# Performance work log

Hardware: AMD Instinct MI355X
Metric: run time of the kernel (lower is better)

## Reference

```python
import jax, jax.numpy as jnp
import numpy as np

N_NODES = 50000
N_EDGES = 800000
F_IN = 64
H1 = 64
H2 = 64
OUT = 8
N_GRAPHS = 128


def gcn_conv(x, W, b, src, dst, n_nodes):
    """PyG GCNConv: sym-normalized aggregation with self-loops.
    out_i = sum_{j->i} d_j^{-1/2} d_i^{-1/2} (x_j W) + d_i^{-1} (x_i W) + b
    where d includes the self-loop (+1)."""
    h = x @ W  # [N, out]
    ones = jnp.ones((src.shape[0],), dtype=x.dtype)
    deg = jnp.zeros((n_nodes,), dtype=x.dtype).at[dst].add(ones) + 1.0  # +1 self-loop
    dinv_sqrt = jax.lax.rsqrt(deg)
    norm = dinv_sqrt[src] * dinv_sqrt[dst]  # [E]
    msgs = h[src] * norm[:, None]  # [E, out] -- dominant memory traffic
    agg = jax.ops.segment_sum(msgs, dst, num_segments=n_nodes)
    agg = agg + h * (1.0 / deg)[:, None]  # self-loop term (norm = 1/d_i)
    return agg + b


def setup_inputs() -> dict:
    key = jax.random.key(0)
    ks = jax.random.split(key, 10)
    x = jax.random.normal(ks[0], (N_NODES, F_IN), dtype=jnp.float32)
    src = jax.random.randint(ks[1], (N_EDGES,), 0, N_NODES, dtype=jnp.int32)
    dst = jax.random.randint(ks[2], (N_EDGES,), 0, N_NODES, dtype=jnp.int32)
    batch = jnp.sort(jax.random.randint(ks[3], (N_NODES,), 0, N_GRAPHS, dtype=jnp.int32))
    s1 = 1.0 / np.sqrt(F_IN)
    s2 = 1.0 / np.sqrt(H1)
    s3 = 1.0 / np.sqrt(H2)
    W1 = jax.random.uniform(ks[4], (F_IN, H1), jnp.float32, -s1, s1)
    b1 = jnp.zeros((H1,), jnp.float32)
    W2 = jax.random.uniform(ks[5], (H1, H2), jnp.float32, -s2, s2)
    b2 = jnp.zeros((H2,), jnp.float32)
    Wfc = jax.random.uniform(ks[6], (H2, OUT), jnp.float32, -s3, s3)
    bfc = jax.random.uniform(ks[7], (OUT,), jnp.float32, -s3, s3)
    return {"x": x, "src": src, "dst": dst, "batch": batch,
            "W1": W1, "b1": b1, "W2": W2, "b2": b2, "Wfc": Wfc, "bfc": bfc}


def reference(x, src, dst, batch, W1, b1, W2, b2, Wfc, bfc):
    n = x.shape[0]
    h = jnp.tanh(gcn_conv(x, W1, b1, src, dst, n))  # dropout(p=0) is identity
    h = jnp.tanh(gcn_conv(h, W2, b2, src, dst, n))
    # global mean pool over graphs
    sums = jax.ops.segment_sum(h, batch, num_segments=N_GRAPHS)  # [G, H2]
    counts = jax.ops.segment_sum(jnp.ones((n,), h.dtype), batch, num_segments=N_GRAPHS)
    pooled = sums / jnp.maximum(counts, 1.0)[:, None]
    return pooled @ Wfc + bfc  # [G, OUT]
```

## Files before the change

### kernel.cpp

```cpp
#include <hip/hip_runtime.h>
#include <hip/hip_fp16.h>
#include <math.h>


#define TPB 256
#define NBIN 256
#define NBLK 256
#define MSZ  (NBIN*NBLK)
#define CAP  4608

#define ADD8(a, v) do { const __half2* _h = (const __half2*)&(v);             \
    float2 _f0 = __half22float2(_h[0]), _f1 = __half22float2(_h[1]);          \
    float2 _f2 = __half22float2(_h[2]), _f3 = __half22float2(_h[3]);          \
    a[0] += _f0.x; a[1] += _f0.y; a[2] += _f1.x; a[3] += _f1.y;               \
    a[4] += _f2.x; a[5] += _f2.y; a[6] += _f3.x; a[7] += _f3.y; } while (0)

__global__ __launch_bounds__(TPB) void k_hist_gemm(const int* __restrict__ dst, int E,
                                                   int* __restrict__ Gh, int binw,
                                                   const float* __restrict__ X,
                                                   const float* __restrict__ W,
                                                   float* __restrict__ Y, int N) {
    if (blockIdx.x < NBIN) {
        __shared__ int hist[NBIN];
        hist[threadIdx.x] = 0;
        __syncthreads();
        int chunk = (E + NBLK - 1) / NBLK;
        int start = blockIdx.x * chunk;
        int end = min(start + chunk, E);
        for (int e = start + threadIdx.x; e < end; e += TPB)
            atomicAdd(&hist[dst[e] / binw], 1);
        __syncthreads();
        Gh[threadIdx.x * NBLK + blockIdx.x] = hist[threadIdx.x];
        return;
    }
    __shared__ float4 Ws[64][16];
    for (int i = threadIdx.x; i < 64 * 16; i += TPB)
        Ws[i >> 4][i & 15] = ((const float4*)W)[i];
    __syncthreads();

    int row = (blockIdx.x - NBIN) * TPB + threadIdx.x;
    if (row >= N) return;
    float xr[64];
    const float4* xp = (const float4*)(X + (size_t)row * 64);
#pragma unroll
    for (int q = 0; q < 16; q++) {
        float4 t = xp[q];
        xr[4 * q + 0] = t.x; xr[4 * q + 1] = t.y;
        xr[4 * q + 2] = t.z; xr[4 * q + 3] = t.w;
    }
    float4 acc[16];
#pragma unroll
    for (int q = 0; q < 16; q++) acc[q] = make_float4(0.f, 0.f, 0.f, 0.f);
#pragma unroll
    for (int k = 0; k < 64; k++) {
        float xk = xr[k];
#pragma unroll
        for (int q = 0; q < 16; q++) {
            float4 w = Ws[k][q];
            acc[q].x += xk * w.x; acc[q].y += xk * w.y;
            acc[q].z += xk * w.z; acc[q].w += xk * w.w;
        }
    }
    float4* yp = (float4*)(Y + (size_t)row * 64);
#pragma unroll
    for (int q = 0; q < 16; q++) yp[q] = acc[q];
}

__global__ __launch_bounds__(1024) void k_scanA(const int* __restrict__ Gh,
                                                int* __restrict__ localex,
                                                int* __restrict__ bsum) {
    __shared__ int buf[1024];
    int i = blockIdx.x * 1024 + threadIdx.x;
    int v = Gh[i];
    buf[threadIdx.x] = v;
    __syncthreads();
#pragma unroll
    for (int off = 1; off < 1024; off <<= 1) {
        int t = (threadIdx.x >= off) ? buf[threadIdx.x - off] : 0;
        __syncthreads();
        buf[threadIdx.x] += t;
        __syncthreads();
    }
    localex[i] = buf[threadIdx.x] - v;
    if (threadIdx.x == 1023) bsum[blockIdx.x] = buf[1023];
}

__global__ __launch_bounds__(1024) void k_scanC(const int* __restrict__ localex,
                                                const int* __restrict__ bsum,
                                                int* __restrict__ Gbase,
                                                int* __restrict__ binptr, int E) {
    __shared__ int offs;
    if (threadIdx.x == 0) {
        int run = 0;
        for (int j = 0; j < (int)blockIdx.x; j++) run += bsum[j];
        offs = run;
    }
    __syncthreads();
    int i = blockIdx.x * 1024 + threadIdx.x;
    int r = localex[i] + offs;
    Gbase[i] = r;
    if ((i & (NBLK - 1)) == 0) binptr[i / NBLK] = r;
    if (i == 0) binptr[NBIN] = E;
}

__global__ __launch_bounds__(TPB) void k_binscatter(const int* __restrict__ src,
                                                    const int* __restrict__ dst,
                                                    const int* __restrict__ Gbase,
                                                    unsigned int* __restrict__ Ebin,
                                                    int E, int binw) {
    __shared__ int curs[NBIN];
    curs[threadIdx.x] = Gbase[threadIdx.x * NBLK + blockIdx.x];
    __syncthreads();
    int chunk = (E + NBLK - 1) / NBLK;
    int start = blockIdx.x * chunk;
    int end = min(start + chunk, E);
    for (int e = start + threadIdx.x; e < end; e += TPB) {
        int d = dst[e], s = src[e];
        int pos = atomicAdd(&curs[d / binw], 1);
        Ebin[pos] = ((unsigned)d << 16) | (unsigned)s;
    }
}

__global__ __launch_bounds__(1024) void k_binsort(const unsigned int* __restrict__ Ebin,
                                                  const int* __restrict__ binptr,
                                                  int* __restrict__ rowptr,
                                                  int* __restrict__ eidx,
                                                  float* __restrict__ ds,
                                                  const float* __restrict__ A,
                                                  __half* __restrict__ Ah,
                                                  int N, int E, int binw) {
    __shared__ unsigned int eLDS[CAP];
    __shared__ int outLDS[CAP];
    __shared__ int hist[NBIN];
    __shared__ int scanb[NBIN];
    __shared__ int curs[NBIN];

    int b = blockIdx.x;
    int base = binptr[b];
    int cntE = min(binptr[b + 1] - base, CAP);
    int nodeBase = b * binw;

    if (threadIdx.x < NBIN) hist[threadIdx.x] = 0;
    __syncthreads();

    for (int j = threadIdx.x; j < cntE; j += 1024) {
        unsigned int u = Ebin[base + j];
        eLDS[j] = u;
        atomicAdd(&hist[(int)(u >> 16) - nodeBase], 1);
    }
    __syncthreads();

    int v = 0;
    if (threadIdx.x < NBIN) { v = hist[threadIdx.x]; scanb[threadIdx.x] = v; }
    __syncthreads();
#pragma unroll
    for (int off = 1; off < NBIN; off <<= 1) {
        int t = (threadIdx.x < NBIN && threadIdx.x >= off) ? scanb[threadIdx.x - off] : 0;
        __syncthreads();
        if (threadIdx.x < NBIN) scanb[threadIdx.x] += t;
        __syncthreads();
    }
    if (threadIdx.x < NBIN) {
        int excl = scanb[threadIdx.x] - v;
        curs[threadIdx.x] = excl;
        int node = nodeBase + threadIdx.x;
        if (threadIdx.x < binw && node < N) {
            rowptr[node] = base + excl;
            ds[node] = rsqrtf((float)v + 1.0f);
        }
    }
    if (b == NBIN - 1 && threadIdx.x == 0) rowptr[N] = E;
    __syncthreads();

    for (int j = threadIdx.x; j < cntE; j += 1024) {
        unsigned int u = eLDS[j];
        int p = atomicAdd(&curs[(int)(u >> 16) - nodeBase], 1);
        outLDS[p] = (int)(u & 0xFFFFu);
    }
    __syncthreads();
    for (int j = threadIdx.x; j < cntE; j += 1024)
        eidx[base + j] = outLDS[j];

    const float2* A2 = (const float2*)A;
    __half2* Ah2 = (__half2*)Ah;
    int total = binw * 32;
    for (int j = threadIdx.x; j < total; j += 1024) {
        int li = j >> 5;
        int node = nodeBase + li;
        if (node >= N) continue;
        float s = rsqrtf((float)hist[li] + 1.0f);
        int c2 = j & 31;
        float2 t = A2[(size_t)node * 32 + c2];
        Ah2[(size_t)node * 32 + c2] = __float22half2_rn(make_float2(t.x * s, t.y * s));
    }
}

__global__ __launch_bounds__(TPB) void k_agg8h(const float4* __restrict__ Hp,
                                               float4* __restrict__ O,
                                               const int* __restrict__ rowptr,
                                               const int* __restrict__ eidx,
                                               const float* __restrict__ ds,
                                               const float* __restrict__ b, int N) {
    int wid = (blockIdx.x * TPB + threadIdx.x) >> 6;
    int lane = threadIdx.x & 63;
    if (wid >= N) return;
    int r = lane >> 3;
    int c = lane & 7;

    int lo = rowptr[wid], hi = rowptr[wid + 1];
    float a[8] = {0.f, 0.f, 0.f, 0.f, 0.f, 0.f, 0.f, 0.f};

    int base = lo;
    for (; base + 16 <= hi; base += 16) {
        int s0 = eidx[base + r], s1 = eidx[base + 8 + r];
        float4 v0 = Hp[(size_t)s0 * 8 + c];
        float4 v1 = Hp[(size_t)s1 * 8 + c];
        ADD8(a, v0);
        ADD8(a, v1);
    }
    if (base + 8 <= hi) {
        int s0 = eidx[base + r];
        float4 v0 = Hp[(size_t)s0 * 8 + c];
        ADD8(a, v0);
        base += 8;
    }
    int rem = hi - base;
    if (r < rem) {
        int s0 = eidx[base + r];
        float4 v0 = Hp[(size_t)s0 * 8 + c];
        ADD8(a, v0);
    }

#pragma unroll
    for (int j = 0; j < 8; j++) a[j] += __shfl_xor(a[j], 8);
#pragma unroll
    for (int j = 0; j < 8; j++) a[j] += __shfl_xor(a[j], 16);
#pragma unroll
    for (int j = 0; j < 8; j++) a[j] += __shfl_xor(a[j], 32);

    if (r == 0) {
        float4 sv = Hp[(size_t)wid * 8 + c];
        ADD8(a, sv);
        float dsd = ds[wid];
        float4 bb0 = ((const float4*)b)[c * 2];
        float4 bb1 = ((const float4*)b)[c * 2 + 1];
        float4 o0, o1;
        o0.x = tanhf(a[0] * dsd + bb0.x);
        o0.y = tanhf(a[1] * dsd + bb0.y);
        o0.z = tanhf(a[2] * dsd + bb0.z);
        o0.w = tanhf(a[3] * dsd + bb0.w);
        o1.x = tanhf(a[4] * dsd + bb1.x);
        o1.y = tanhf(a[5] * dsd + bb1.y);
        o1.z = tanhf(a[6] * dsd + bb1.z);
        o1.w = tanhf(a[7] * dsd + bb1.w);
        O[(size_t)wid * 16 + c * 2] = o0;
        O[(size_t)wid * 16 + c * 2 + 1] = o1;
    }
}

__global__ __launch_bounds__(TPB) void k_gemm64h(const float* __restrict__ X,
                                                 const float* __restrict__ W,
                                                 __half* __restrict__ Ah, int N,
                                                 const float* __restrict__ ds) {
    __shared__ float4 Ws[64][16];
    for (int i = threadIdx.x; i < 64 * 16; i += TPB)
        Ws[i >> 4][i & 15] = ((const float4*)W)[i];
    __syncthreads();

    int row = blockIdx.x * TPB + threadIdx.x;
    if (row >= N) return;
    float xr[64];
    const float4* xp = (const float4*)(X + (size_t)row * 64);
#pragma unroll
    for (int q = 0; q < 16; q++) {
        float4 t = xp[q];
        xr[4 * q + 0] = t.x; xr[4 * q + 1] = t.y;
        xr[4 * q + 2] = t.z; xr[4 * q + 3] = t.w;
    }
    float4 acc[16];
#pragma unroll
    for (int q = 0; q < 16; q++) acc[q] = make_float4(0.f, 0.f, 0.f, 0.f);
#pragma unroll
    for (int k = 0; k < 64; k++) {
        float xk = xr[k];
#pragma unroll
        for (int q = 0; q < 16; q++) {
            float4 w = Ws[k][q];
            acc[q].x += xk * w.x; acc[q].y += xk * w.y;
            acc[q].z += xk * w.z; acc[q].w += xk * w.w;
        }
    }
    float s = ds[row];
    __half2* yh = (__half2*)(Ah + (size_t)row * 64);
#pragma unroll
    for (int q = 0; q < 16; q++) {
        yh[2 * q]     = __float22half2_rn(make_float2(acc[q].x * s, acc[q].y * s));
        yh[2 * q + 1] = __float22half2_rn(make_float2(acc[q].z * s, acc[q].w * s));
    }
}

__global__ __launch_bounds__(TPB) void k_poolfc(const float* __restrict__ H,
                                                const int* __restrict__ batch,
                                                const float* __restrict__ Wfc,
                                                const float* __restrict__ bfc,
                                                float* __restrict__ out, int N) {
    int g = blockIdx.x;
    __shared__ int range[2];
    __shared__ float red[4][64];
    if (threadIdx.x == 0) {
        int lo = 0, hi = N;
        while (lo < hi) { int m = (lo + hi) >> 1; if (batch[m] < g) lo = m + 1; else hi = m; }
        range[0] = lo;
        hi = N;
        while (lo < hi) { int m = (lo + hi) >> 1; if (batch[m] < g + 1) lo = m + 1; else hi = m; }
        range[1] = lo;
    }
    __syncthreads();
    int lo = range[0], hi = range[1];
    int wid = threadIdx.x >> 6, lane = threadIdx.x & 63;

    float acc = 0.0f;
    for (int n = lo + wid; n < hi; n += 4) acc += H[(size_t)n * 64 + lane];
    red[wid][lane] = acc;
    __syncthreads();
    if (wid == 0) {
        float s = red[0][lane] + red[1][lane] + red[2][lane] + red[3][lane];
        float cgt = fmaxf((float)(hi - lo), 1.0f);
        red[0][lane] = s / cgt;
    }
    __syncthreads();
    if (threadIdx.x < 8) {
        int o = threadIdx.x;
        float accf = bfc[o];
#pragma unroll
        for (int f = 0; f < 64; f++) accf += red[0][f] * Wfc[f * 8 + o];
        out[g * 8 + o] = accf;
    }
}

extern "C" void kernel_launch(void* const* d_in, const int* in_sizes, int n_in,
                              void* d_out, int out_size, void* d_ws, size_t ws_size,
                              hipStream_t stream) {
    const float* x     = (const float*)d_in[0];
    const int*   src   = (const int*)d_in[1];
    const int*   dst   = (const int*)d_in[2];
    const int*   batch = (const int*)d_in[3];
    const float* W1    = (const float*)d_in[4];
    const float* b1    = (const float*)d_in[5];
    const float* W2    = (const float*)d_in[6];
    const float* b2    = (const float*)d_in[7];
    const float* Wfc   = (const float*)d_in[8];
    const float* bfc   = (const float*)d_in[9];
    float* out = (float*)d_out;

    const int N = in_sizes[0] / 64;
    const int E = in_sizes[1];
    const int G = out_size / 8;
    const int binw = (N + NBIN - 1) / NBIN;

    const size_t NB = (size_t)N * 64 * sizeof(float);
    char* ws = (char*)d_ws;
    size_t off = 0;
    float* A      = (float*)(ws + off); off += NB;
    float* B      = (float*)(ws + off); off += NB;
    unsigned int* Ebin = (unsigned int*)B;
    __half* Ah    = (__half*)(ws + off); off += NB / 2;
    int*   eidx   = (int*)(ws + off);   off += (size_t)E * 4;
    int*   Gh     = (int*)(ws + off);   off += (size_t)MSZ * 4;
    int*   localx = (int*)(ws + off);   off += (size_t)MSZ * 4;
    int*   Gbase  = (int*)(ws + off);   off += (size_t)MSZ * 4;
    int*   binptr = (int*)(ws + off);   off += (size_t)(NBIN + 1) * 4;
    int*   bsum   = (int*)(ws + off);   off += 256;
    int*   rowptr = (int*)(ws + off);   off += (size_t)(N + 1) * 4;
    float* dsv    = (float*)(ws + off); off += (size_t)N * 4;

    const int gN = (N + TPB - 1) / TPB;
    const int gW = (N * 64 + TPB - 1) / TPB;

    k_hist_gemm<<<NBIN + gN, TPB, 0, stream>>>(dst, E, Gh, binw, x, W1, A, N);
    k_scanA<<<MSZ / 1024, 1024, 0, stream>>>(Gh, localx, bsum);
    k_scanC<<<MSZ / 1024, 1024, 0, stream>>>(localx, bsum, Gbase, binptr, E);
    k_binscatter<<<NBLK, TPB, 0, stream>>>(src, dst, Gbase, Ebin, E, binw);
    k_binsort<<<NBIN, 1024, 0, stream>>>(Ebin, binptr, rowptr, eidx, dsv, A, Ah, N, E, binw);

    k_agg8h<<<gW, TPB, 0, stream>>>((const float4*)Ah, (float4*)B, rowptr, eidx, dsv, b1, N);
    k_gemm64h<<<gN, TPB, 0, stream>>>(B, W2, Ah, N, dsv);
    k_agg8h<<<gW, TPB, 0, stream>>>((const float4*)Ah, (float4*)B, rowptr, eidx, dsv, b2, N);
    k_poolfc<<<G, TPB, 0, stream>>>(B, batch, Wfc, bfc, out, N);
}
```

Before: 155.6 us.

## Store layer activations in fp16 and merge two-pass scan into one kernel

The aggregation kernel now writes its tanh outputs as packed half precision instead of fp32. The following GEMM and the pooling kernel read these fp16 activations, which halves the intermediate traffic. Separately, the two scan kernels are merged into one: each block recomputes its prefix by reducing all earlier histogram entries, which removes a launch and the localex/bsum round trip at the cost of redundant reads. The fp16 storage adds rounding error to the intermediate activations.

```diff
diff --git a/kernel.cpp b/kernel.cpp
--- a/kernel.cpp
+++ b/kernel.cpp
@@ -66,11 +66,27 @@
     for (int q = 0; q < 16; q++) yp[q] = acc[q];
 }
 
-__global__ __launch_bounds__(1024) void k_scanA(const int* __restrict__ Gh,
-                                                int* __restrict__ localex,
-                                                int* __restrict__ bsum) {
+__global__ __launch_bounds__(1024) void k_scan(const int* __restrict__ Gh,
+                                               int* __restrict__ Gbase,
+                                               int* __restrict__ binptr, int E) {
     __shared__ int buf[1024];
-    int i = blockIdx.x * 1024 + threadIdx.x;
+    __shared__ int bprefix;
+    int blk = blockIdx.x;
+
+    int limit = blk * 1024;
+    int part = 0;
+    for (int j = threadIdx.x; j < limit; j += 1024) part += Gh[j];
+    buf[threadIdx.x] = part;
+    __syncthreads();
+#pragma unroll
+    for (int off = 512; off > 0; off >>= 1) {
+        if (threadIdx.x < off) buf[threadIdx.x] += buf[threadIdx.x + off];
+        __syncthreads();
+    }
+    if (threadIdx.x == 0) bprefix = buf[0];
+    __syncthreads();
+
+    int i = blk * 1024 + threadIdx.x;
     int v = Gh[i];
     buf[threadIdx.x] = v;
     __syncthreads();
@@ -81,23 +97,7 @@
         buf[threadIdx.x] += t;
         __syncthreads();
     }
-    localex[i] = buf[threadIdx.x] - v;
-    if (threadIdx.x == 1023) bsum[blockIdx.x] = buf[1023];
-}
-
-__global__ __launch_bounds__(1024) void k_scanC(const int* __restrict__ localex,
-                                                const int* __restrict__ bsum,
-                                                int* __restrict__ Gbase,
-                                                int* __restrict__ binptr, int E) {
-    __shared__ int offs;
-    if (threadIdx.x == 0) {
-        int run = 0;
-        for (int j = 0; j < (int)blockIdx.x; j++) run += bsum[j];
-        offs = run;
-    }
-    __syncthreads();
-    int i = blockIdx.x * 1024 + threadIdx.x;
-    int r = localex[i] + offs;
+    int r = buf[threadIdx.x] - v + bprefix;
     Gbase[i] = r;
     if ((i & (NBLK - 1)) == 0) binptr[i / NBLK] = r;
     if (i == 0) binptr[NBIN] = E;
@@ -196,7 +196,7 @@
 }
 
 __global__ __launch_bounds__(TPB) void k_agg8h(const float4* __restrict__ Hp,
-                                               float4* __restrict__ O,
+                                               float4* __restrict__ Oh,
                                                const int* __restrict__ rowptr,
                                                const int* __restrict__ eidx,
                                                const float* __restrict__ ds,
@@ -244,21 +244,25 @@
         float dsd = ds[wid];
         float4 bb0 = ((const float4*)b)[c * 2];
         float4 bb1 = ((const float4*)b)[c * 2 + 1];
-        float4 o0, o1;
-        o0.x = tanhf(a[0] * dsd + bb0.x);
-        o0.y = tanhf(a[1] * dsd + bb0.y);
-        o0.z = tanhf(a[2] * dsd + bb0.z);
-        o0.w = tanhf(a[3] * dsd + bb0.w);
-        o1.x = tanhf(a[4] * dsd + bb1.x);
-        o1.y = tanhf(a[5] * dsd + bb1.y);
-        o1.z = tanhf(a[6] * dsd + bb1.z);
-        o1.w = tanhf(a[7] * dsd + bb1.w);
-        O[(size_t)wid * 16 + c * 2] = o0;
-        O[(size_t)wid * 16 + c * 2 + 1] = o1;
-    }
-}
-
-__global__ __launch_bounds__(TPB) void k_gemm64h(const float* __restrict__ X,
+        float o0 = tanhf(a[0] * dsd + bb0.x);
+        float o1 = tanhf(a[1] * dsd + bb0.y);
+        float o2 = tanhf(a[2] * dsd + bb0.z);
+        float o3 = tanhf(a[3] * dsd + bb0.w);
+        float o4 = tanhf(a[4] * dsd + bb1.x);
+        float o5 = tanhf(a[5] * dsd + bb1.y);
+        float o6 = tanhf(a[6] * dsd + bb1.z);
+        float o7 = tanhf(a[7] * dsd + bb1.w);
+        float4 pk;
+        __half2* ph = (__half2*)&pk;
+        ph[0] = __float22half2_rn(make_float2(o0, o1));
+        ph[1] = __float22half2_rn(make_float2(o2, o3));
+        ph[2] = __float22half2_rn(make_float2(o4, o5));
+        ph[3] = __float22half2_rn(make_float2(o6, o7));
+        Oh[(size_t)wid * 8 + c] = pk;
+    }
+}
+
+__global__ __launch_bounds__(TPB) void k_gemm64h(const __half* __restrict__ Xh,
                                                  const float* __restrict__ W,
                                                  __half* __restrict__ Ah, int N,
                                                  const float* __restrict__ ds) {
@@ -270,12 +274,17 @@
     int row = blockIdx.x * TPB + threadIdx.x;
     if (row >= N) return;
     float xr[64];
-    const float4* xp = (const float4*)(X + (size_t)row * 64);
-#pragma unroll
-    for (int q = 0; q < 16; q++) {
+    const float4* xp = (const float4*)(Xh + (size_t)row * 64);
+#pragma unroll
+    for (int q = 0; q < 8; q++) {
         float4 t = xp[q];
-        xr[4 * q + 0] = t.x; xr[4 * q + 1] = t.y;
-        xr[4 * q + 2] = t.z; xr[4 * q + 3] = t.w;
+        const __half2* h = (const __half2*)&t;
+        float2 f0 = __half22float2(h[0]), f1 = __half22float2(h[1]);
+        float2 f2 = __half22float2(h[2]), f3 = __half22float2(h[3]);
+        xr[8 * q + 0] = f0.x; xr[8 * q + 1] = f0.y;
+        xr[8 * q + 2] = f1.x; xr[8 * q + 3] = f1.y;
+        xr[8 * q + 4] = f2.x; xr[8 * q + 5] = f2.y;
+        xr[8 * q + 6] = f3.x; xr[8 * q + 7] = f3.y;
     }
     float4 acc[16];
 #pragma unroll
@@ -299,7 +308,7 @@
     }
 }
 
-__global__ __launch_bounds__(TPB) void k_poolfc(const float* __restrict__ H,
+__global__ __launch_bounds__(TPB) void k_poolfc(const __half* __restrict__ H,
                                                 const int* __restrict__ batch,
                                                 const float* __restrict__ Wfc,
                                                 const float* __restrict__ bfc,
@@ -320,7 +329,7 @@
     int wid = threadIdx.x >> 6, lane = threadIdx.x & 63;
 
     float acc = 0.0f;
-    for (int n = lo + wid; n < hi; n += 4) acc += H[(size_t)n * 64 + lane];
+    for (int n = lo + wid; n < hi; n += 4) acc += __half2float(H[(size_t)n * 64 + lane]);
     red[wid][lane] = acc;
     __syncthreads();
     if (wid == 0) {
@@ -361,16 +370,15 @@
     const size_t NB = (size_t)N * 64 * sizeof(float);
     char* ws = (char*)d_ws;
     size_t off = 0;
-    float* A      = (float*)(ws + off); off += NB;
-    float* B      = (float*)(ws + off); off += NB;
-    unsigned int* Ebin = (unsigned int*)B;
-    __half* Ah    = (__half*)(ws + off); off += NB / 2;
+    float*  A    = (float*)(ws + off);  off += NB;
+    __half* Ah   = (__half*)(ws + off); off += NB / 2;
+    __half* Bh   = (__half*)(ws + off); off += NB / 2;
+    unsigned int* Ebin = (unsigned int*)Bh;
+    __half* B2h  = (__half*)(ws + off); off += NB / 2;
     int*   eidx   = (int*)(ws + off);   off += (size_t)E * 4;
     int*   Gh     = (int*)(ws + off);   off += (size_t)MSZ * 4;
-    int*   localx = (int*)(ws + off);   off += (size_t)MSZ * 4;
     int*   Gbase  = (int*)(ws + off);   off += (size_t)MSZ * 4;
     int*   binptr = (int*)(ws + off);   off += (size_t)(NBIN + 1) * 4;
-    int*   bsum   = (int*)(ws + off);   off += 256;
     int*   rowptr = (int*)(ws + off);   off += (size_t)(N + 1) * 4;
     float* dsv    = (float*)(ws + off); off += (size_t)N * 4;
 
@@ -378,13 +386,12 @@
     const int gW = (N * 64 + TPB - 1) / TPB;
 
     k_hist_gemm<<<NBIN + gN, TPB, 0, stream>>>(dst, E, Gh, binw, x, W1, A, N);
-    k_scanA<<<MSZ / 1024, 1024, 0, stream>>>(Gh, localx, bsum);
-    k_scanC<<<MSZ / 1024, 1024, 0, stream>>>(localx, bsum, Gbase, binptr, E);
+    k_scan<<<MSZ / 1024, 1024, 0, stream>>>(Gh, Gbase, binptr, E);
     k_binscatter<<<NBLK, TPB, 0, stream>>>(src, dst, Gbase, Ebin, E, binw);
     k_binsort<<<NBIN, 1024, 0, stream>>>(Ebin, binptr, rowptr, eidx, dsv, A, Ah, N, E, binw);
 
-    k_agg8h<<<gW, TPB, 0, stream>>>((const float4*)Ah, (float4*)B, rowptr, eidx, dsv, b1, N);
-    k_gemm64h<<<gN, TPB, 0, stream>>>(B, W2, Ah, N, dsv);
-    k_agg8h<<<gW, TPB, 0, stream>>>((const float4*)Ah, (float4*)B, rowptr, eidx, dsv, b2, N);
-    k_poolfc<<<G, TPB, 0, stream>>>(B, batch, Wfc, bfc, out, N);
-}
+    k_agg8h<<<gW, TPB, 0, stream>>>((const float4*)Ah, (float4*)Bh, rowptr, eidx, dsv, b1, N);
+    k_gemm64h<<<gN, TPB, 0, stream>>>(Bh, W2, Ah, N, dsv);
+    k_agg8h<<<gW, TPB, 0, stream>>>((const float4*)Ah, (float4*)B2h, rowptr, eidx, dsv, b2, N);
+    k_poolfc<<<G, TPB, 0, stream>>>(B2h, batch, Wfc, bfc, out, N);
+}
```

Measured after the change: 163.3 us. 1.05x slower.
